# Kernel tuning notes

Hardware: AMD Instinct MI355X
Metric: run time of the kernel (lower is better)

The kernel has to match this reference:

```python
import jax, jax.numpy as jnp
import numpy as np

BN_EPS = 1e-6


def setup_inputs() -> dict:
    key = jax.random.key(0)
    ks = jax.random.split(key, 6)
    B, N, K, D = 4, 40960, 16, 8
    coords = jax.random.normal(ks[0], (B, N, 3), dtype=jnp.float32)
    features = jax.random.normal(ks[1], (B, D, N, 1), dtype=jnp.float32)
    idx = jax.random.randint(ks[2], (B, N, K), 0, N, dtype=jnp.int32)
    dist = jax.random.uniform(ks[3], (B, N, K), dtype=jnp.float32)
    W = jax.random.normal(ks[4], (D, 10), dtype=jnp.float32) * 0.3
    b = jax.random.normal(ks[5], (D,), dtype=jnp.float32) * 0.1
    gamma = jnp.ones((D,), dtype=jnp.float32)
    beta = jnp.zeros((D,), dtype=jnp.float32)
    return {"coords": coords, "features": features, "idx": idx, "dist": dist,
            "W": W, "b": b, "gamma": gamma, "beta": beta}


def _locse(coords, features, idx, dist, W, b, gamma, beta):
    B, N, K = idx.shape
    D = W.shape[0]
    # gather neighbor coords: [B,N,K,3]
    neighbors = jax.vmap(lambda c, i: c[i])(coords, idx)
    center = jnp.broadcast_to(coords[:, :, None, :], (B, N, K, 3))
    # 10-channel relative-position encoding, channels-last [B,N,K,10]
    concat = jnp.concatenate(
        [center, neighbors, center - neighbors, dist[..., None]], axis=-1)
    # 1x1 conv (10 -> d), output [B,D,N,K]
    h = jnp.einsum('bnkc,dc->bdnk', concat, W) + b[None, :, None, None]
    # BatchNorm2d (training-mode batch stats over B,N,K per channel), eps=1e-6
    mean = jnp.mean(h, axis=(0, 2, 3), keepdims=True)
    var = jnp.var(h, axis=(0, 2, 3), keepdims=True)
    h = (h - mean) * jax.lax.rsqrt(var + BN_EPS)
    h = h * gamma[None, :, None, None] + beta[None, :, None, None]
    h = jax.nn.relu(h)
    # concat with broadcast input features -> [B, 2D, N, K]
    feats = jnp.broadcast_to(features, (B, D, N, K))
    return jnp.concatenate([h, feats], axis=1)


def reference(coords, features, idx, dist, W, b, gamma, beta):
    return _locse(coords, features, idx, dist, W, b, gamma, beta)
```

## Files before the change

### kernel.cpp

```cpp
#include <hip/hip_runtime.h>
#include <hip/hip_bf16.h>

constexpr int BB = 4;
constexpr int NN = 40960;
constexpr int KK = 16;
constexpr int DD = 8;
constexpr float BN_EPS = 1e-6f;

constexpr int STATS_BLOCKS = 2048;
constexpr int STATS_THREADS = 256;

constexpr int C4_FLOATS = BB * NN * 4;

__global__ __launch_bounds__(256) void locse_pad_coords_kernel(
    const float* __restrict__ coords, float* __restrict__ coords4)
{
    const int i = blockIdx.x * blockDim.x + threadIdx.x;
    if (i < BB * NN) {
        const float* c = coords + (size_t)i * 3;
        float4 v = make_float4(c[0], c[1], c[2], 0.f);
        *reinterpret_cast<float4*>(coords4 + (size_t)i * 4) = v;
    }
}

__global__ __launch_bounds__(STATS_THREADS) void locse_stats_kernel(
    const float* __restrict__ coords4, const int* __restrict__ idx,
    const float* __restrict__ dist, const float* __restrict__ W,
    const float* __restrict__ bias, float* __restrict__ partials)
{
    __shared__ float sW[80];
    __shared__ float sb[8];
    if (threadIdx.x < 80) sW[threadIdx.x] = W[threadIdx.x];
    if (threadIdx.x < 8)  sb[threadIdx.x] = bias[threadIdx.x];
    __syncthreads();

    float sum[8] = {0.f, 0.f, 0.f, 0.f, 0.f, 0.f, 0.f, 0.f};
    float sq[8]  = {0.f, 0.f, 0.f, 0.f, 0.f, 0.f, 0.f, 0.f};

    const int total4 = BB * NN * (KK / 4);
    for (int t = blockIdx.x * blockDim.x + threadIdx.x; t < total4;
         t += gridDim.x * blockDim.x) {
        const int k4 = t & 3;
        const int bn = t >> 2;
        const int b  = bn / NN;
        const float4 cc =
            *reinterpret_cast<const float4*>(coords4 + (size_t)bn * 4);
        const float cx = cc.x, cy = cc.y, cz = cc.z;

        const int base = (bn << 4) + (k4 << 2);
        const int4   j4 = *reinterpret_cast<const int4*>(idx + base);
        const float4 d4 = *reinterpret_cast<const float4*>(dist + base);
        const int   js[4] = {j4.x, j4.y, j4.z, j4.w};
        const float ds[4] = {d4.x, d4.y, d4.z, d4.w};

        #pragma unroll
        for (int kk = 0; kk < 4; ++kk) {
            const float4 nc = *reinterpret_cast<const float4*>(
                coords4 + ((size_t)b * NN + js[kk]) * 4);
            const float nx = nc.x, ny = nc.y, nz = nc.z;
            const float c10[10] = {cx, cy, cz, nx, ny, nz,
                                   cx - nx, cy - ny, cz - nz, ds[kk]};
            #pragma unroll
            for (int d = 0; d < 8; ++d) {
                float h = sb[d];
                #pragma unroll
                for (int c = 0; c < 10; ++c) h = fmaf(sW[d * 10 + c], c10[c], h);
                sum[d] += h;
                sq[d]  += h * h;
            }
        }
    }

    #pragma unroll
    for (int v = 0; v < 8; ++v) {
        float s = sum[v], q = sq[v];
        #pragma unroll
        for (int off = 32; off > 0; off >>= 1) {
            s += __shfl_down(s, off, 64);
            q += __shfl_down(q, off, 64);
        }
        sum[v] = s; sq[v] = q;
    }

    __shared__ float wred[STATS_THREADS / 64][16];
    const int lane = threadIdx.x & 63;
    const int wid  = threadIdx.x >> 6;
    if (lane == 0) {
        #pragma unroll
        for (int v = 0; v < 8; ++v) {
            wred[wid][v]     = sum[v];
            wred[wid][8 + v] = sq[v];
        }
    }
    __syncthreads();
    if (threadIdx.x < 16) {
        float s = 0.f;
        #pragma unroll
        for (int w = 0; w < STATS_THREADS / 64; ++w) s += wred[w][threadIdx.x];
        partials[blockIdx.x * 16 + threadIdx.x] = s;
    }
}

__global__ __launch_bounds__(256) void locse_finalize_kernel(
    const float* __restrict__ partials, const float* __restrict__ W,
    const float* __restrict__ bias, const float* __restrict__ gamma,
    const float* __restrict__ beta, float* __restrict__ wp,
    float* __restrict__ bp)
{
    const int t = threadIdx.x;
    const int c = t & 15;
    float acc = 0.f;
    for (int i = t >> 4; i < STATS_BLOCKS; i += 16) acc += partials[i * 16 + c];

    __shared__ float red[256];
    __shared__ float tot[16];
    __shared__ float scale_s[8];
    red[t] = acc;
    __syncthreads();
    if (t < 16) {
        float s = 0.f;
        #pragma unroll
        for (int i = 0; i < 16; ++i) s += red[i * 16 + t];
        tot[t] = s;
    }
    __syncthreads();
    if (t < 8) {
        const float cnt  = (float)BB * (float)NN * (float)KK;
        const float mean = tot[t] / cnt;
        const float var  = tot[8 + t] / cnt - mean * mean;
        const float sc   = gamma[t] * rsqrtf(var + BN_EPS);
        scale_s[t] = sc;
        bp[t] = fmaf(bias[t] - mean, sc, beta[t]);
    }
    __syncthreads();
    if (t < 80) wp[t] = W[t] * scale_s[t / 10];
}

__global__ __launch_bounds__(256) void locse_out_kernel(
    const float* __restrict__ coords4, const float* __restrict__ features,
    const int* __restrict__ idx, const float* __restrict__ dist,
    const float* __restrict__ wp, const float* __restrict__ bp,
    float* __restrict__ out)
{
    __shared__ float sW[80];
    __shared__ float sb[8];
    if (threadIdx.x < 80) sW[threadIdx.x] = wp[threadIdx.x];
    if (threadIdx.x < 8)  sb[threadIdx.x] = bp[threadIdx.x];
    __syncthreads();

    const int total4 = BB * NN * (KK / 4);
    for (int t = blockIdx.x * blockDim.x + threadIdx.x; t < total4;
         t += gridDim.x * blockDim.x) {
        const int k4 = t & 3;
        const int bn = t >> 2;
        const int n  = bn % NN;
        const int b  = bn / NN;
        const float4 cc =
            *reinterpret_cast<const float4*>(coords4 + (size_t)bn * 4);
        const float cx = cc.x, cy = cc.y, cz = cc.z;

        const int base = (bn << 4) + (k4 << 2);
        const int4   j4 = *reinterpret_cast<const int4*>(idx + base);
        const float4 d4 = *reinterpret_cast<const float4*>(dist + base);
        const int   js[4] = {j4.x, j4.y, j4.z, j4.w};
        const float ds[4] = {d4.x, d4.y, d4.z, d4.w};

        float hv[8][4];
        #pragma unroll
        for (int kk = 0; kk < 4; ++kk) {
            const float4 nc = *reinterpret_cast<const float4*>(
                coords4 + ((size_t)b * NN + js[kk]) * 4);
            const float nx = nc.x, ny = nc.y, nz = nc.z;
            const float c10[10] = {cx, cy, cz, nx, ny, nz,
                                   cx - nx, cy - ny, cz - nz, ds[kk]};
            #pragma unroll
            for (int d = 0; d < 8; ++d) {
                float h = sb[d];
                #pragma unroll
                for (int c = 0; c < 10; ++c) h = fmaf(sW[d * 10 + c], c10[c], h);
                hv[d][kk] = fmaxf(h, 0.f);
            }
        }

        const size_t outn = (size_t)b * 16 * NN * KK + (size_t)n * KK + (k4 << 2);
        #pragma unroll
        for (int d = 0; d < 8; ++d) {
            *reinterpret_cast<float4*>(out + outn + (size_t)d * NN * KK) =
                make_float4(hv[d][0], hv[d][1], hv[d][2], hv[d][3]);
        }
        #pragma unroll
        for (int d = 0; d < 8; ++d) {
            const float f = features[((size_t)b * DD + d) * NN + n];
            *reinterpret_cast<float4*>(out + outn + (size_t)(8 + d) * NN * KK) =
                make_float4(f, f, f, f);
        }
    }
}

extern "C" void kernel_launch(void* const* d_in, const int* in_sizes, int n_in,
                              void* d_out, int out_size, void* d_ws, size_t ws_size,
                              hipStream_t stream) {
    const float* coords   = (const float*)d_in[0];
    const float* features = (const float*)d_in[1];
    const int*   idx      = (const int*)d_in[2];
    const float* dist     = (const float*)d_in[3];
    const float* W        = (const float*)d_in[4];
    const float* bias     = (const float*)d_in[5];
    const float* gamma    = (const float*)d_in[6];
    const float* beta     = (const float*)d_in[7];
    float* out = (float*)d_out;

    float* wsf      = (float*)d_ws;
    float* coords4  = wsf;
    float* partials = wsf + C4_FLOATS;
    float* wp       = partials + STATS_BLOCKS * 16;
    float* bp       = wp + 80;

    const int npts = BB * NN;
    locse_pad_coords_kernel<<<dim3((npts + 255) / 256), dim3(256), 0, stream>>>(
        coords, coords4);
    locse_stats_kernel<<<dim3(STATS_BLOCKS), dim3(STATS_THREADS), 0, stream>>>(
        coords4, idx, dist, W, bias, partials);
    locse_finalize_kernel<<<dim3(1), dim3(256), 0, stream>>>(
        partials, W, bias, gamma, beta, wp, bp);

    const int total4 = BB * NN * (KK / 4);
    const int blocks = (total4 + 255) / 256;
    locse_out_kernel<<<dim3(blocks), dim3(256), 0, stream>>>(
        coords4, features, idx, dist, wp, bp, out);
}
```

Baseline: 283.3 us.

## Store unnormalized conv output in stats pass and normalize in place afterward

The statistics kernel now writes the pre-normalization conv results into the output buffer while it accumulates the sums. A lightweight apply kernel then reads them back, applies the per-channel scale and shift with ReLU, and writes the broadcast features. This removes the second round of neighbor gathers and the 10x8 matvec recompute, but adds an extra write and read of half the output tensor.

```diff
diff --git a/kernel.cpp b/kernel.cpp
--- a/kernel.cpp
+++ b/kernel.cpp
@@ -23,10 +23,11 @@
     }
 }
 
-__global__ __launch_bounds__(STATS_THREADS) void locse_stats_kernel(
+__global__ __launch_bounds__(STATS_THREADS) void locse_stats_h_kernel(
     const float* __restrict__ coords4, const int* __restrict__ idx,
     const float* __restrict__ dist, const float* __restrict__ W,
-    const float* __restrict__ bias, float* __restrict__ partials)
+    const float* __restrict__ bias, float* __restrict__ partials,
+    float* __restrict__ out)
 {
     __shared__ float sW[80];
     __shared__ float sb[8];
@@ -42,6 +43,7 @@
          t += gridDim.x * blockDim.x) {
         const int k4 = t & 3;
         const int bn = t >> 2;
+        const int n  = bn % NN;
         const int b  = bn / NN;
         const float4 cc =
             *reinterpret_cast<const float4*>(coords4 + (size_t)bn * 4);
@@ -53,6 +55,7 @@
         const int   js[4] = {j4.x, j4.y, j4.z, j4.w};
         const float ds[4] = {d4.x, d4.y, d4.z, d4.w};
 
+        float hv[8][4];
         #pragma unroll
         for (int kk = 0; kk < 4; ++kk) {
             const float4 nc = *reinterpret_cast<const float4*>(
@@ -65,9 +68,17 @@
                 float h = sb[d];
                 #pragma unroll
                 for (int c = 0; c < 10; ++c) h = fmaf(sW[d * 10 + c], c10[c], h);
+                hv[d][kk] = h;
                 sum[d] += h;
                 sq[d]  += h * h;
             }
+        }
+
+        const size_t outn = (size_t)b * 16 * NN * KK + (size_t)n * KK + (k4 << 2);
+        #pragma unroll
+        for (int d = 0; d < 8; ++d) {
+            *reinterpret_cast<float4*>(out + outn + (size_t)d * NN * KK) =
+                make_float4(hv[d][0], hv[d][1], hv[d][2], hv[d][3]);
         }
     }
 
@@ -102,10 +113,8 @@
 }
 
 __global__ __launch_bounds__(256) void locse_finalize_kernel(
-    const float* __restrict__ partials, const float* __restrict__ W,
-    const float* __restrict__ bias, const float* __restrict__ gamma,
-    const float* __restrict__ beta, float* __restrict__ wp,
-    float* __restrict__ bp)
+    const float* __restrict__ partials, const float* __restrict__ gamma,
+    const float* __restrict__ beta, float* __restrict__ scsh)
 {
     const int t = threadIdx.x;
     const int c = t & 15;
@@ -114,7 +123,6 @@
 
     __shared__ float red[256];
     __shared__ float tot[16];
-    __shared__ float scale_s[8];
     red[t] = acc;
     __syncthreads();
     if (t < 16) {
@@ -129,71 +137,47 @@
         const float mean = tot[t] / cnt;
         const float var  = tot[8 + t] / cnt - mean * mean;
         const float sc   = gamma[t] * rsqrtf(var + BN_EPS);
-        scale_s[t] = sc;
-        bp[t] = fmaf(bias[t] - mean, sc, beta[t]);
-    }
-    __syncthreads();
-    if (t < 80) wp[t] = W[t] * scale_s[t / 10];
-}
-
-__global__ __launch_bounds__(256) void locse_out_kernel(
-    const float* __restrict__ coords4, const float* __restrict__ features,
-    const int* __restrict__ idx, const float* __restrict__ dist,
-    const float* __restrict__ wp, const float* __restrict__ bp,
+        scsh[t]     = sc;
+        scsh[8 + t] = beta[t] - mean * sc;
+    }
+}
+
+__global__ __launch_bounds__(256) void locse_apply_kernel(
+    const float* __restrict__ features, const float* __restrict__ scsh,
     float* __restrict__ out)
 {
-    __shared__ float sW[80];
-    __shared__ float sb[8];
-    if (threadIdx.x < 80) sW[threadIdx.x] = wp[threadIdx.x];
-    if (threadIdx.x < 8)  sb[threadIdx.x] = bp[threadIdx.x];
+    __shared__ float ssc[8];
+    __shared__ float ssh[8];
+    if (threadIdx.x < 8)  ssc[threadIdx.x] = scsh[threadIdx.x];
+    else if (threadIdx.x < 16) ssh[threadIdx.x - 8] = scsh[threadIdx.x];
     __syncthreads();
 
     const int total4 = BB * NN * (KK / 4);
-    for (int t = blockIdx.x * blockDim.x + threadIdx.x; t < total4;
-         t += gridDim.x * blockDim.x) {
-        const int k4 = t & 3;
-        const int bn = t >> 2;
-        const int n  = bn % NN;
-        const int b  = bn / NN;
-        const float4 cc =
-            *reinterpret_cast<const float4*>(coords4 + (size_t)bn * 4);
-        const float cx = cc.x, cy = cc.y, cz = cc.z;
-
-        const int base = (bn << 4) + (k4 << 2);
-        const int4   j4 = *reinterpret_cast<const int4*>(idx + base);
-        const float4 d4 = *reinterpret_cast<const float4*>(dist + base);
-        const int   js[4] = {j4.x, j4.y, j4.z, j4.w};
-        const float ds[4] = {d4.x, d4.y, d4.z, d4.w};
-
-        float hv[8][4];
-        #pragma unroll
-        for (int kk = 0; kk < 4; ++kk) {
-            const float4 nc = *reinterpret_cast<const float4*>(
-                coords4 + ((size_t)b * NN + js[kk]) * 4);
-            const float nx = nc.x, ny = nc.y, nz = nc.z;
-            const float c10[10] = {cx, cy, cz, nx, ny, nz,
-                                   cx - nx, cy - ny, cz - nz, ds[kk]};
-            #pragma unroll
-            for (int d = 0; d < 8; ++d) {
-                float h = sb[d];
-                #pragma unroll
-                for (int c = 0; c < 10; ++c) h = fmaf(sW[d * 10 + c], c10[c], h);
-                hv[d][kk] = fmaxf(h, 0.f);
-            }
-        }
-
-        const size_t outn = (size_t)b * 16 * NN * KK + (size_t)n * KK + (k4 << 2);
-        #pragma unroll
-        for (int d = 0; d < 8; ++d) {
-            *reinterpret_cast<float4*>(out + outn + (size_t)d * NN * KK) =
-                make_float4(hv[d][0], hv[d][1], hv[d][2], hv[d][3]);
-        }
-        #pragma unroll
-        for (int d = 0; d < 8; ++d) {
-            const float f = features[((size_t)b * DD + d) * NN + n];
-            *reinterpret_cast<float4*>(out + outn + (size_t)(8 + d) * NN * KK) =
-                make_float4(f, f, f, f);
-        }
+    const int t = blockIdx.x * blockDim.x + threadIdx.x;
+    if (t >= total4) return;
+
+    const int k4 = t & 3;
+    const int bn = t >> 2;
+    const int n  = bn % NN;
+    const int b  = bn / NN;
+
+    const size_t outn = (size_t)b * 16 * NN * KK + (size_t)n * KK + (k4 << 2);
+    #pragma unroll
+    for (int d = 0; d < 8; ++d) {
+        float4* p = reinterpret_cast<float4*>(out + outn + (size_t)d * NN * KK);
+        float4 h = *p;
+        const float sc = ssc[d], sh = ssh[d];
+        h.x = fmaxf(fmaf(h.x, sc, sh), 0.f);
+        h.y = fmaxf(fmaf(h.y, sc, sh), 0.f);
+        h.z = fmaxf(fmaf(h.z, sc, sh), 0.f);
+        h.w = fmaxf(fmaf(h.w, sc, sh), 0.f);
+        *p = h;
+    }
+    #pragma unroll
+    for (int d = 0; d < 8; ++d) {
+        const float f = features[((size_t)b * DD + d) * NN + n];
+        *reinterpret_cast<float4*>(out + outn + (size_t)(8 + d) * NN * KK) =
+            make_float4(f, f, f, f);
     }
 }
 
@@ -213,19 +197,18 @@
     float* wsf      = (float*)d_ws;
     float* coords4  = wsf;
     float* partials = wsf + C4_FLOATS;
-    float* wp       = partials + STATS_BLOCKS * 16;
-    float* bp       = wp + 80;
+    float* scsh     = partials + STATS_BLOCKS * 16;
 
     const int npts = BB * NN;
     locse_pad_coords_kernel<<<dim3((npts + 255) / 256), dim3(256), 0, stream>>>(
         coords, coords4);
-    locse_stats_kernel<<<dim3(STATS_BLOCKS), dim3(STATS_THREADS), 0, stream>>>(
-        coords4, idx, dist, W, bias, partials);
+    locse_stats_h_kernel<<<dim3(STATS_BLOCKS), dim3(STATS_THREADS), 0, stream>>>(
+        coords4, idx, dist, W, bias, partials, out);
     locse_finalize_kernel<<<dim3(1), dim3(256), 0, stream>>>(
-        partials, W, bias, gamma, beta, wp, bp);
+        partials, gamma, beta, scsh);
 
     const int total4 = BB * NN * (KK / 4);
     const int blocks = (total4 + 255) / 256;
-    locse_out_kernel<<<dim3(blocks), dim3(256), 0, stream>>>(
-        coords4, features, idx, dist, wp, bp, out);
-}
+    locse_apply_kernel<<<dim3(blocks), dim3(256), 0, stream>>>(
+        features, scsh, out);
+}
```

New measurement: 294.4 us. 3.9% more time.
